# Kernel tuning notes

Measured on AMD Instinct MI355X. Metric: run time of the kernel, lower is better.

## Reference

```python
import math
import jax, jax.numpy as jnp
import numpy as np

B, S, E, H = 4, 1024, 768, 12
HD = E // H
NUM_BUCKETS, MAX_DIST = 320, 800


def setup_inputs() -> dict:
    key = jax.random.key(0)
    ks = jax.random.split(key, 8)
    w = lambda k, sh: jax.random.normal(k, sh, jnp.float32) * 0.02
    return {
        "hidden_states": jax.random.normal(ks[0], (B, S, E), jnp.float32),
        "q_w": w(ks[1], (E, E)), "q_b": jnp.zeros((E,), jnp.float32),
        "k_w": w(ks[2], (E, E)), "k_b": jnp.zeros((E,), jnp.float32),
        "v_w": w(ks[3], (E, E)), "v_b": jnp.zeros((E,), jnp.float32),
        "out_w": w(ks[4], (E, E)), "out_b": jnp.zeros((E,), jnp.float32),
        "gru_const": jnp.ones((1, H, 1, 1), jnp.float32),
        "gru_w": w(ks[5], (8, HD)), "gru_b": jnp.zeros((8,), jnp.float32),
        "rel_embed": w(ks[6], (NUM_BUCKETS, H)),
    }


def _relative_positions_bucket(rel):
    # rel: (S, S) int32, rel = memory_pos - context_pos
    nb = NUM_BUCKETS // 2
    buckets = (rel > 0).astype(jnp.int32) * nb
    rel = jnp.abs(rel)
    max_exact = nb // 2
    is_small = rel < max_exact
    large = jnp.log(rel.astype(jnp.float32) / max_exact)
    large = large / math.log(MAX_DIST / max_exact) * (nb - max_exact)
    large = (max_exact + large).astype(jnp.int32)
    large = jnp.minimum(large, nb - 1)
    return buckets + jnp.where(is_small, rel, large)


def _compute_position_bias(rel_embed):
    pos = jnp.arange(S, dtype=jnp.int32)
    rel = pos[None, :] - pos[:, None]              # (S, S)
    bucket = _relative_positions_bucket(rel)       # (S, S) int32
    return rel_embed[bucket].transpose(2, 0, 1)    # (H, S, S)


def reference(hidden_states, q_w, q_b, k_w, k_b, v_w, v_b, out_w, out_b,
              gru_const, gru_w, gru_b, rel_embed):
    position_bias = _compute_position_bias(rel_embed)          # (H, S, S)

    # gated relative-position bias
    ghs = hidden_states.reshape(B, S, H, HD).transpose(0, 2, 1, 3)   # (B,H,S,HD)
    proj = jnp.einsum("bhsd,ed->bhse", ghs, gru_w) + gru_b           # (B,H,S,8)
    proj = proj.reshape(B, H, S, 2, 4).sum(-1)                       # (B,H,S,2)
    gates = jax.nn.sigmoid(proj)
    gate_a, gate_b = gates[..., 0:1], gates[..., 1:2]                # (B,H,S,1)
    gate = gate_a * (gate_b * gru_const - 1.0) + 2.0                 # (B,H,S,1)
    gated_bias = gate[..., None, :, 0][..., None] * 0  # placeholder removed below
    gated_bias = gate * position_bias[None]                          # (B,H,S,S)

    scaling = HD ** -0.5
    q = (hidden_states @ q_w.T + q_b).reshape(B, S, H, HD).transpose(0, 2, 1, 3) * scaling
    k = (hidden_states @ k_w.T + k_b).reshape(B, S, H, HD).transpose(0, 2, 1, 3)
    v = (hidden_states @ v_w.T + v_b).reshape(B, S, H, HD).transpose(0, 2, 1, 3)

    scores = jnp.einsum("bhqd,bhkd->bhqk", q, k) + gated_bias
    attn = jax.nn.softmax(scores, axis=-1)
    ctx = jnp.einsum("bhqk,bhkd->bhqd", attn, v)                     # (B,H,S,HD)
    ctx = ctx.transpose(0, 2, 1, 3).reshape(B, S, E)
    attn_output = ctx @ out_w.T + out_b
    return attn_output, position_bias
```

## Files before the change

### kernel.cpp

```cpp
#include <hip/hip_runtime.h>

typedef unsigned short u16;
typedef __attribute__((ext_vector_type(4))) unsigned short u16x4;
typedef __attribute__((ext_vector_type(8))) short s8v;
typedef __attribute__((ext_vector_type(4))) float f4v;

#define BB 4
#define SS 1024
#define EE 768
#define HH 12
#define DD 64

#define NHS (BB * SS * EE)
#define NW  (EE * EE)
#define LOG2E 1.4426950408889634f

static __device__ __forceinline__ u16 f2bf(float x){
  unsigned int u = __float_as_uint(x);
  u += 0x7fffu + ((u >> 16) & 1u);
  return (u16)(u >> 16);
}
static __device__ __forceinline__ unsigned cvt_pk_bf16(float lo, float hi){
  unsigned r;
  asm("v_cvt_pk_bf16_f32 %0, %1, %2" : "=v"(r) : "v"(lo), "v"(hi));
  return r;
}
static __device__ __forceinline__ void stage16(const u16* g, u16* l){
  __builtin_amdgcn_global_load_lds(
      (const __attribute__((address_space(1))) void*)g,
      (__attribute__((address_space(3))) void*)l, 16, 0, 0);
}

__global__ __launch_bounds__(256) void cvt_kernel(const float* __restrict__ hs,
                                                  const float* __restrict__ qw,
                                                  const float* __restrict__ kw,
                                                  const float* __restrict__ vw,
                                                  const float* __restrict__ ow,
                                                  u16* __restrict__ dst){
  size_t e = ((size_t)blockIdx.x * 256 + threadIdx.x) * 8;
  const float* src;
  if      (e < (size_t)NHS)            src = hs + e;
  else if (e < (size_t)NHS + NW)       src = qw + (e - NHS);
  else if (e < (size_t)NHS + 2 * NW)   src = kw + (e - NHS - NW);
  else if (e < (size_t)NHS + 3 * NW)   src = vw + (e - NHS - 2 * (size_t)NW);
  else                                 src = ow + (e - NHS - 3 * (size_t)NW);
  f4v v0 = *(const f4v*)src, v1 = *(const f4v*)(src + 4);
  s8v o;
  #pragma unroll
  for (int i = 0; i < 4; i++){ o[i] = (short)f2bf(v0[i]); o[4 + i] = (short)f2bf(v1[i]); }
  size_t row = e / EE;
  int k = (int)(e - row * EE);
  size_t d = row * EE + (size_t)(k ^ (((int)row & 7) << 3));
  *(s8v*)(dst + d) = o;
}

__global__ __launch_bounds__(256) void tbl_kernel(const float* __restrict__ rel_embed,
                                                  float* __restrict__ tbl){
  int id = blockIdx.x * 256 + threadIdx.x;
  int h = id >> 11, r = id & 2047;
  float v = 0.f;
  if (r < 2047){
    int rel = r - 1023;
    int bucket = (rel > 0) ? 160 : 0;
    int a = rel < 0 ? -rel : rel;
    int idx;
    if (a < 80) idx = a;
    else {
      float t = logf((float)a / 80.0f);
      t = t / 2.302585092994046f * 80.0f;
      int lg = (int)(80.0f + t);
      idx = lg < 159 ? lg : 159;
    }
    v = rel_embed[(idx + bucket) * HH + h];
  }
  tbl[id] = v;
}

__global__ __launch_bounds__(256) void pb_kernel(const float* __restrict__ tbl,
                                                 float* __restrict__ pb){
  int id = blockIdx.x * 256 + threadIdx.x;
  int i = id >> 8, j = (id & 255) * 4;
  int base = j - i + 1023;
  #pragma unroll
  for (int h = 0; h < HH; h++){
    const float* th = tbl + h * 2048;
    f4v v;
    #pragma unroll
    for (int jj = 0; jj < 4; jj++) v[jj] = th[base + jj];
    __builtin_nontemporal_store(v, (f4v*)&pb[(size_t)h * (SS * SS) + (size_t)i * SS + j]);
  }
}

__global__ __launch_bounds__(256) void gate_kernel(const float* __restrict__ hs,
                                                   const float* __restrict__ gru_w,
                                                   const float* __restrict__ gru_b,
                                                   const float* __restrict__ gru_c,
                                                   float* __restrict__ gate){
  int wid = blockIdx.x * 4 + (threadIdx.x >> 6);
  int lane = threadIdx.x & 63;
  int s = wid & (SS - 1);
  int bh = wid >> 10;
  int h = bh % HH, b = bh / HH;
  float x = hs[(size_t)(b * SS + s) * EE + h * DD + lane];
  float w0 = gru_w[lane] + gru_w[64 + lane] + gru_w[128 + lane] + gru_w[192 + lane];
  float w1 = gru_w[256 + lane] + gru_w[320 + lane] + gru_w[384 + lane] + gru_w[448 + lane];
  float y0 = x * w0, y1 = x * w1;
  #pragma unroll
  for (int off = 1; off < 64; off <<= 1){
    y0 += __shfl_xor(y0, off);
    y1 += __shfl_xor(y1, off);
  }
  if (lane == 0){
    float s0 = y0 + gru_b[0] + gru_b[1] + gru_b[2] + gru_b[3];
    float s1 = y1 + gru_b[4] + gru_b[5] + gru_b[6] + gru_b[7];
    float ga = 1.f / (1.f + __expf(-s0));
    float gb = 1.f / (1.f + __expf(-s1));
    gate[wid] = ga * (gb * gru_c[h] - 1.0f) + 2.0f;
  }
}

template<int EP>
static __device__ __forceinline__ void gemm_body(const u16* __restrict__ A,
                                                 const u16* __restrict__ Bw,
                                                 const float* __restrict__ bias,
                                                 void* __restrict__ Cp,
                                                 float scale, int m0, int n0){
  __shared__ __align__(16) u16 a_s[128 * 64];
  __shared__ __align__(16) u16 b_s[128 * 64];
  const int t = threadIdx.x;
  const int wave = t >> 6, lane = t & 63;
  const int lr = lane & 15, lg = lane >> 4;
  const int wm = (wave >> 1) * 64, wn = (wave & 1) * 64;
  const int srow = lane >> 3;
  const int scol = (lane & 7) * 8;
  const int swz = (lr & 7) << 3;

  const f4v zero = {0.f, 0.f, 0.f, 0.f};
  f4v acc[4][4];
  #pragma unroll
  for (int i = 0; i < 4; i++)
    #pragma unroll
    for (int j = 0; j < 4; j++) acc[i][j] = zero;

  for (int k0 = 0; k0 < EE; k0 += 64){
    if (k0) __syncthreads();
    #pragma unroll
    for (int i = 0; i < 4; i++){
      const int chunk = i * 4 + wave;
      const int r = chunk * 8 + srow;
      stage16(A  + (size_t)(m0 + r) * EE + k0 + scol, &a_s[chunk * 512]);
      stage16(Bw + (size_t)(n0 + r) * EE + k0 + scol, &b_s[chunk * 512]);
    }
    __syncthreads();
    #pragma unroll
    for (int kk = 0; kk < 2; kk++){
      const int cbase = (kk * 32 + lg * 8) ^ swz;
      s8v af[4], bf[4];
      #pragma unroll
      for (int i = 0; i < 4; i++){
        af[i] = *(const s8v*)&a_s[(wm + i * 16 + lr) * 64 + cbase];
        bf[i] = *(const s8v*)&b_s[(wn + i * 16 + lr) * 64 + cbase];
      }
      #pragma unroll
      for (int i = 0; i < 4; i++)
        #pragma unroll
        for (int j = 0; j < 4; j++)
          acc[i][j] = __builtin_amdgcn_mfma_f32_16x16x32_bf16(af[i], bf[j], acc[i][j], 0, 0, 0);
    }
  }

  #pragma unroll
  for (int ii = 0; ii < 4; ii++){
    const int row0 = m0 + wm + ii * 16 + lg * 4;
    const int bb = row0 >> 10;
    const int s0 = row0 & (SS - 1);
    #pragma unroll
    for (int j = 0; j < 4; j++){
      const int col = n0 + wn + j * 16 + lr;
      const float bv = bias[col];
      if (EP == 0){
        const int h = col >> 6, dim = col & 63;
        const int bh = bb * HH + h;
        u16* dst = (u16*)Cp + ((size_t)((bh * 64 + (s0 >> 4)) * 2 + (dim >> 5))) * 512
                   + ((dim >> 3) & 3) * 128 + (s0 & 15) * 8 + (dim & 7);
        #pragma unroll
        for (int r = 0; r < 4; r++)
          dst[r * 8] = f2bf((acc[ii][j][r] + bv) * scale);
      } else if (EP == 2){
        const int h = col >> 6, dim = col & 63;
        const int bh = bb * HH + h;
        u16x4 pk;
        #pragma unroll
        for (int r = 0; r < 4; r++) pk[r] = f2bf(acc[ii][j][r] + bv);
        *(u16x4*)((u16*)Cp + ((size_t)(((bh * 16 + (s0 >> 6)) * 2 + ((s0 >> 5) & 1)) * 4 + (dim >> 4))) * 512
                  + ((s0 >> 3) & 3) * 128 + (dim & 15) * 8 + (s0 & 7)) = pk;
      } else {
        #pragma unroll
        for (int r = 0; r < 4; r++)
          ((float*)Cp)[(size_t)(row0 + r) * EE + col] = acc[ii][j][r] + bv;
      }
    }
  }
}

__global__ __launch_bounds__(256) void gemm_qkv(const u16* __restrict__ A,
                                                const u16* __restrict__ wqkv,
                                                const float* __restrict__ bq,
                                                const float* __restrict__ bk,
                                                const float* __restrict__ bv,
                                                u16* __restrict__ qo,
                                                u16* __restrict__ ko,
                                                u16* __restrict__ vo){
  const int z = blockIdx.z;
  if (z == 2)
    gemm_body<2>(A, wqkv + 2 * (size_t)NW, bv, vo, 1.0f, blockIdx.x * 128, blockIdx.y * 128);
  else
    gemm_body<0>(A, wqkv + (size_t)z * NW, z ? bk : bq, z ? ko : qo,
                 z ? 1.0f : 0.125f * LOG2E, blockIdx.x * 128, blockIdx.y * 128);
}

__global__ __launch_bounds__(256) void gemm_out(const u16* __restrict__ A,
                                                const u16* __restrict__ Bw,
                                                const float* __restrict__ bias,
                                                float* __restrict__ Cp){
  gemm_body<1>(A, Bw, bias, Cp, 1.0f, blockIdx.x * 128, blockIdx.y * 128);
}

__global__ __launch_bounds__(256) void attn_kernel(const u16* __restrict__ qpack,
                                                   const u16* __restrict__ kpack,
                                                   const u16* __restrict__ vpack,
                                                   const float* __restrict__ gate,
                                                   const float* __restrict__ tbl,
                                                   u16* __restrict__ ctx){
  __shared__ __align__(16) float tbl_s[2048];
  __shared__ __align__(16) u16 kv_s[2][8192];
  __shared__ __align__(16) u16 p_s[4][16][72];
  const int t = threadIdx.x, wave = t >> 6, lane = t & 63;
  const int lr = lane & 15, lg = lane >> 4;
  const int h = blockIdx.y, b = blockIdx.z;
  const int bh = b * HH + h;
  const int q0w = blockIdx.x * 64 + wave * 16;
  {
    const float* th = tbl + h * 2048 + t * 8;
    *(f4v*)&tbl_s[t * 8]     = *(const f4v*)th;
    *(f4v*)&tbl_s[t * 8 + 4] = *(const f4v*)(th + 4);
  }
  const u16* qp = qpack + ((size_t)(bh * 64 + blockIdx.x * 4 + wave)) * 1024 + lane * 8;
  const s8v qf0 = *(const s8v*)qp;
  const s8v qf1 = *(const s8v*)(qp + 512);
  const float gt = gate[(size_t)bh * SS + q0w + lr] * LOG2E;

  const u16* kbase = kpack + (size_t)bh * 65536;
  const u16* vbase = vpack + (size_t)bh * 65536;
  const int so = wave * 1024 + lane * 8;

  stage16(kbase + so,        &kv_s[0][wave * 1024]);
  stage16(kbase + so + 512,  &kv_s[0][wave * 1024 + 512]);
  stage16(vbase + so,        &kv_s[0][4096 + wave * 1024]);
  stage16(vbase + so + 512,  &kv_s[0][4096 + wave * 1024 + 512]);
  __syncthreads();

  const f4v zero = {0.f, 0.f, 0.f, 0.f};
  f4v o[4];
  #pragma unroll
  for (int d = 0; d < 4; d++) o[d] = zero;
  float m = -1e30f, l = 0.f;
  const int tb_off = 1023 - q0w;
  const int voff = lg * 4 - lr;

  for (int kt = 0; kt < 16; kt++){
    const int cur = kt & 1;
    if (kt < 15){
      const u16* kg = kbase + (kt + 1) * 4096;
      const u16* vg = vbase + (kt + 1) * 4096;
      u16* kl = &kv_s[cur ^ 1][wave * 1024];
      u16* vl = &kv_s[cur ^ 1][4096 + wave * 1024];
      stage16(kg + so,       kl);
      stage16(kg + so + 512, kl + 512);
      stage16(vg + so,       vl);
      stage16(vg + so + 512, vl + 512);
    }
    const u16* kl = &kv_s[cur][0];
    const u16* vl = &kv_s[cur][4096];
    s8v kf0[4], kf1[4], vf0[4], vf1[4];
    #pragma unroll
    for (int n = 0; n < 4; n++){
      kf0[n] = *(const s8v*)&kl[n * 1024 + lane * 8];
      kf1[n] = *(const s8v*)&kl[n * 1024 + 512 + lane * 8];
    }
    #pragma unroll
    for (int d = 0; d < 4; d++){
      vf0[d] = *(const s8v*)&vl[d * 512 + lane * 8];
      vf1[d] = *(const s8v*)&vl[2048 + d * 512 + lane * 8];
    }
    f4v sf[4];
    __builtin_amdgcn_s_setprio(1);
    #pragma unroll
    for (int n = 0; n < 4; n++){
      f4v z = zero;
      z = __builtin_amdgcn_mfma_f32_16x16x32_bf16(kf0[n], qf0, z, 0, 0, 0);
      z = __builtin_amdgcn_mfma_f32_16x16x32_bf16(kf1[n], qf1, z, 0, 0, 0);
      sf[n] = z;
    }
    __builtin_amdgcn_s_setprio(0);
    #pragma unroll
    for (int n = 0; n < 4; n++){
      const float* tp = &tbl_s[kt * 64 + n * 16 + tb_off + voff];
      #pragma unroll
      for (int r = 0; r < 4; r++)
        sf[n][r] += gt * tp[r];
    }
    float lm = fmaxf(fmaxf(fmaxf(sf[0][0], sf[0][1]), fmaxf(sf[0][2], sf[0][3])),
                     fmaxf(fmaxf(sf[1][0], sf[1][1]), fmaxf(sf[1][2], sf[1][3])));
    lm = fmaxf(lm, fmaxf(fmaxf(fmaxf(sf[2][0], sf[2][1]), fmaxf(sf[2][2], sf[2][3])),
                         fmaxf(fmaxf(sf[3][0], sf[3][1]), fmaxf(sf[3][2], sf[3][3]))));
    if (__any(lm - m > 8.0f)){
      float gm = fmaxf(lm, __shfl_xor(lm, 16));
      gm = fmaxf(gm, __shfl_xor(gm, 32));
      float nm = fmaxf(m, gm);
      float sc = exp2f(m - nm);
      m = nm;
      l *= sc;
      float scq[4];
      #pragma unroll
      for (int r = 0; r < 4; r++) scq[r] = __shfl(sc, lg * 4 + r);
      #pragma unroll
      for (int d = 0; d < 4; d++)
        #pragma unroll
        for (int r = 0; r < 4; r++) o[d][r] *= scq[r];
    }
    float ps = 0.f;
    #pragma unroll
    for (int n = 0; n < 4; n++){
      #pragma unroll
      for (int r = 0; r < 4; r++){
        float p = exp2f(sf[n][r] - m);
        sf[n][r] = p;
        ps += p;
      }
    }
    l += ps;
    #pragma unroll
    for (int n = 0; n < 4; n++){
      unsigned pk0 = cvt_pk_bf16(sf[n][0], sf[n][1]);
      unsigned pk1 = cvt_pk_bf16(sf[n][2], sf[n][3]);
      u16* prow = &p_s[wave][lr][n * 16 + lg * 4];
      *(unsigned*)prow       = pk0;
      *(unsigned*)(prow + 2) = pk1;
    }
    const s8v pf0 = *(const s8v*)&p_s[wave][lr][lg * 8];
    const s8v pf1 = *(const s8v*)&p_s[wave][lr][32 + lg * 8];
    __builtin_amdgcn_s_setprio(1);
    #pragma unroll
    for (int d = 0; d < 4; d++){
      o[d] = __builtin_amdgcn_mfma_f32_16x16x32_bf16(pf0, vf0[d], o[d], 0, 0, 0);
      o[d] = __builtin_amdgcn_mfma_f32_16x16x32_bf16(pf1, vf1[d], o[d], 0, 0, 0);
    }
    __builtin_amdgcn_s_setprio(0);
    __syncthreads();
  }
  l += __shfl_xor(l, 16);
  l += __shfl_xor(l, 32);
  float rl = 1.0f / l;
  float linv[4];
  #pragma unroll
  for (int r = 0; r < 4; r++) linv[r] = __shfl(rl, lg * 4 + r);
  #pragma unroll
  for (int d = 0; d < 4; d++)
    #pragma unroll
    for (int r = 0; r < 4; r++){
      float val = o[d][r] * linv[r];
      const int row = q0w + lg * 4 + r;
      const int col = (h * DD + d * 16 + lr) ^ ((row & 7) << 3);
      ctx[(size_t)(b * SS + row) * EE + col] = f2bf(val);
    }
}

extern "C" void kernel_launch(void* const* d_in, const int* in_sizes, int n_in,
                              void* d_out, int out_size, void* d_ws, size_t ws_size,
                              hipStream_t stream){
  const float* hs    = (const float*)d_in[0];
  const float* q_w   = (const float*)d_in[1];
  const float* q_b   = (const float*)d_in[2];
  const float* k_w   = (const float*)d_in[3];
  const float* k_b   = (const float*)d_in[4];
  const float* v_w   = (const float*)d_in[5];
  const float* v_b   = (const float*)d_in[6];
  const float* o_w   = (const float*)d_in[7];
  const float* o_b   = (const float*)d_in[8];
  const float* gru_c = (const float*)d_in[9];
  const float* gru_w = (const float*)d_in[10];
  const float* gru_b = (const float*)d_in[11];
  const float* rel   = (const float*)d_in[12];

  float* out0 = (float*)d_out;
  float* pb   = out0 + (size_t)BB * SS * EE;

  char* w = (char*)d_ws;
  u16* qpk  = (u16*)w;  w += (size_t)NHS * 2;
  u16* kpk  = (u16*)w;  w += (size_t)NHS * 2;
  u16* vpk  = (u16*)w;  w += (size_t)NHS * 2;
  u16* cvt  = (u16*)w;  w += ((size_t)NHS + 4 * (size_t)NW) * 2;
  float* gate = (float*)w; w += (size_t)BB * HH * SS * 4;
  float* tbl  = (float*)w;

  u16* hs_bf  = cvt;
  u16* wqkv   = cvt + NHS;
  u16* ow_bf  = cvt + NHS + 3 * (size_t)NW;

  cvt_kernel<<<(NHS + 4 * NW) / (256 * 8), 256, 0, stream>>>(hs, q_w, k_w, v_w, o_w, cvt);
  tbl_kernel<<<(HH * 2048) / 256, 256, 0, stream>>>(rel, tbl);
  gate_kernel<<<(BB * HH * SS) / 4, 256, 0, stream>>>(hs, gru_w, gru_b, gru_c, gate);
  gemm_qkv<<<dim3(32, 6, 3), 256, 0, stream>>>(hs_bf, wqkv, q_b, k_b, v_b, qpk, kpk, vpk);
  attn_kernel<<<dim3(SS / 64, HH, BB), 256, 0, stream>>>(qpk, kpk, vpk, gate, tbl, hs_bf);
  gemm_out<<<dim3(32, 6), 256, 0, stream>>>(hs_bf, ow_bf, o_b, out0);
  pb_kernel<<<(SS * SS / 4) / 256, 256, 0, stream>>>(tbl, pb);
}
```

Measured before the change: 116.5 us.

## Merge prep kernels and fuse position-bias output write into attention epilogue

```diff
diff --git a/kernel.cpp b/kernel.cpp
--- a/kernel.cpp
+++ b/kernel.cpp
@@ -31,91 +31,76 @@
       (__attribute__((address_space(3))) void*)l, 16, 0, 0);
 }
 
-__global__ __launch_bounds__(256) void cvt_kernel(const float* __restrict__ hs,
-                                                  const float* __restrict__ qw,
-                                                  const float* __restrict__ kw,
-                                                  const float* __restrict__ vw,
-                                                  const float* __restrict__ ow,
-                                                  u16* __restrict__ dst){
-  size_t e = ((size_t)blockIdx.x * 256 + threadIdx.x) * 8;
-  const float* src;
-  if      (e < (size_t)NHS)            src = hs + e;
-  else if (e < (size_t)NHS + NW)       src = qw + (e - NHS);
-  else if (e < (size_t)NHS + 2 * NW)   src = kw + (e - NHS - NW);
-  else if (e < (size_t)NHS + 3 * NW)   src = vw + (e - NHS - 2 * (size_t)NW);
-  else                                 src = ow + (e - NHS - 3 * (size_t)NW);
-  f4v v0 = *(const f4v*)src, v1 = *(const f4v*)(src + 4);
-  s8v o;
-  #pragma unroll
-  for (int i = 0; i < 4; i++){ o[i] = (short)f2bf(v0[i]); o[4 + i] = (short)f2bf(v1[i]); }
-  size_t row = e / EE;
-  int k = (int)(e - row * EE);
-  size_t d = row * EE + (size_t)(k ^ (((int)row & 7) << 3));
-  *(s8v*)(dst + d) = o;
-}
-
-__global__ __launch_bounds__(256) void tbl_kernel(const float* __restrict__ rel_embed,
-                                                  float* __restrict__ tbl){
-  int id = blockIdx.x * 256 + threadIdx.x;
-  int h = id >> 11, r = id & 2047;
-  float v = 0.f;
-  if (r < 2047){
-    int rel = r - 1023;
-    int bucket = (rel > 0) ? 160 : 0;
-    int a = rel < 0 ? -rel : rel;
-    int idx;
-    if (a < 80) idx = a;
-    else {
-      float t = logf((float)a / 80.0f);
-      t = t / 2.302585092994046f * 80.0f;
-      int lg = (int)(80.0f + t);
-      idx = lg < 159 ? lg : 159;
-    }
-    v = rel_embed[(idx + bucket) * HH + h];
-  }
-  tbl[id] = v;
-}
-
-__global__ __launch_bounds__(256) void pb_kernel(const float* __restrict__ tbl,
-                                                 float* __restrict__ pb){
-  int id = blockIdx.x * 256 + threadIdx.x;
-  int i = id >> 8, j = (id & 255) * 4;
-  int base = j - i + 1023;
-  #pragma unroll
-  for (int h = 0; h < HH; h++){
-    const float* th = tbl + h * 2048;
-    f4v v;
-    #pragma unroll
-    for (int jj = 0; jj < 4; jj++) v[jj] = th[base + jj];
-    __builtin_nontemporal_store(v, (f4v*)&pb[(size_t)h * (SS * SS) + (size_t)i * SS + j]);
-  }
-}
-
-__global__ __launch_bounds__(256) void gate_kernel(const float* __restrict__ hs,
+__global__ __launch_bounds__(256) void prep_kernel(const float* __restrict__ hs,
+                                                   const float* __restrict__ qw,
+                                                   const float* __restrict__ kw,
+                                                   const float* __restrict__ vw,
+                                                   const float* __restrict__ ow,
+                                                   u16* __restrict__ dst,
+                                                   const float* __restrict__ rel_embed,
+                                                   float* __restrict__ tbl,
                                                    const float* __restrict__ gru_w,
                                                    const float* __restrict__ gru_b,
                                                    const float* __restrict__ gru_c,
                                                    float* __restrict__ gate){
-  int wid = blockIdx.x * 4 + (threadIdx.x >> 6);
-  int lane = threadIdx.x & 63;
-  int s = wid & (SS - 1);
-  int bh = wid >> 10;
-  int h = bh % HH, b = bh / HH;
-  float x = hs[(size_t)(b * SS + s) * EE + h * DD + lane];
-  float w0 = gru_w[lane] + gru_w[64 + lane] + gru_w[128 + lane] + gru_w[192 + lane];
-  float w1 = gru_w[256 + lane] + gru_w[320 + lane] + gru_w[384 + lane] + gru_w[448 + lane];
-  float y0 = x * w0, y1 = x * w1;
-  #pragma unroll
-  for (int off = 1; off < 64; off <<= 1){
-    y0 += __shfl_xor(y0, off);
-    y1 += __shfl_xor(y1, off);
-  }
-  if (lane == 0){
-    float s0 = y0 + gru_b[0] + gru_b[1] + gru_b[2] + gru_b[3];
-    float s1 = y1 + gru_b[4] + gru_b[5] + gru_b[6] + gru_b[7];
-    float ga = 1.f / (1.f + __expf(-s0));
-    float gb = 1.f / (1.f + __expf(-s1));
-    gate[wid] = ga * (gb * gru_c[h] - 1.0f) + 2.0f;
+  const int bid = blockIdx.x;
+  if (bid < 2688){
+    size_t e = ((size_t)bid * 256 + threadIdx.x) * 8;
+    const float* src;
+    if      (e < (size_t)NHS)            src = hs + e;
+    else if (e < (size_t)NHS + NW)       src = qw + (e - NHS);
+    else if (e < (size_t)NHS + 2 * NW)   src = kw + (e - NHS - NW);
+    else if (e < (size_t)NHS + 3 * NW)   src = vw + (e - NHS - 2 * (size_t)NW);
+    else                                 src = ow + (e - NHS - 3 * (size_t)NW);
+    f4v v0 = *(const f4v*)src, v1 = *(const f4v*)(src + 4);
+    s8v o;
+    #pragma unroll
+    for (int i = 0; i < 4; i++){ o[i] = (short)f2bf(v0[i]); o[4 + i] = (short)f2bf(v1[i]); }
+    size_t row = e / EE;
+    int k = (int)(e - row * EE);
+    size_t d = row * EE + (size_t)(k ^ (((int)row & 7) << 3));
+    *(s8v*)(dst + d) = o;
+  } else if (bid < 2784){
+    int id = (bid - 2688) * 256 + threadIdx.x;
+    int h = id >> 11, r = id & 2047;
+    float v = 0.f;
+    if (r < 2047){
+      int rel = r - 1023;
+      int bucket = (rel > 0) ? 160 : 0;
+      int a = rel < 0 ? -rel : rel;
+      int idx;
+      if (a < 80) idx = a;
+      else {
+        float t = logf((float)a / 80.0f);
+        t = t / 2.302585092994046f * 80.0f;
+        int lg = (int)(80.0f + t);
+        idx = lg < 159 ? lg : 159;
+      }
+      v = rel_embed[(idx + bucket) * HH + h];
+    }
+    tbl[id] = v;
+  } else {
+    int wid = (bid - 2784) * 4 + (threadIdx.x >> 6);
+    int lane = threadIdx.x & 63;
+    int s = wid & (SS - 1);
+    int bh = wid >> 10;
+    int h = bh % HH, b = bh / HH;
+    float x = hs[(size_t)(b * SS + s) * EE + h * DD + lane];
+    float w0 = gru_w[lane] + gru_w[64 + lane] + gru_w[128 + lane] + gru_w[192 + lane];
+    float w1 = gru_w[256 + lane] + gru_w[320 + lane] + gru_w[384 + lane] + gru_w[448 + lane];
+    float y0 = x * w0, y1 = x * w1;
+    #pragma unroll
+    for (int off = 1; off < 64; off <<= 1){
+      y0 += __shfl_xor(y0, off);
+      y1 += __shfl_xor(y1, off);
+    }
+    if (lane == 0){
+      float s0 = y0 + gru_b[0] + gru_b[1] + gru_b[2] + gru_b[3];
+      float s1 = y1 + gru_b[4] + gru_b[5] + gru_b[6] + gru_b[7];
+      float ga = 1.f / (1.f + __expf(-s0));
+      float gb = 1.f / (1.f + __expf(-s1));
+      gate[wid] = ga * (gb * gru_c[h] - 1.0f) + 2.0f;
+    }
   }
 }
 
@@ -231,7 +216,8 @@
                                                    const u16* __restrict__ vpack,
                                                    const float* __restrict__ gate,
                                                    const float* __restrict__ tbl,
-                                                   u16* __restrict__ ctx){
+                                                   u16* __restrict__ ctx,
+                                                   float* __restrict__ pb){
   __shared__ __align__(16) float tbl_s[2048];
   __shared__ __align__(16) u16 kv_s[2][8192];
   __shared__ __align__(16) u16 p_s[4][16][72];
@@ -374,6 +360,21 @@
       const int col = (h * DD + d * 16 + lr) ^ ((row & 7) << 3);
       ctx[(size_t)(b * SS + row) * EE + col] = f2bf(val);
     }
+  {
+    float* pbh = pb + (size_t)h * (SS * SS);
+    const int i0 = (blockIdx.x * 4 + b) * 16;
+    #pragma unroll 4
+    for (int rr = 0; rr < 16; rr++){
+      const int i = i0 + rr;
+      const int base = 1023 - i + t * 4;
+      f4v v;
+      v[0] = tbl_s[base + 0];
+      v[1] = tbl_s[base + 1];
+      v[2] = tbl_s[base + 2];
+      v[3] = tbl_s[base + 3];
+      __builtin_nontemporal_store(v, (f4v*)&pbh[(size_t)i * SS + t * 4]);
+    }
+  }
 }
 
 extern "C" void kernel_launch(void* const* d_in, const int* in_sizes, int n_in,
@@ -408,11 +409,9 @@
   u16* wqkv   = cvt + NHS;
   u16* ow_bf  = cvt + NHS + 3 * (size_t)NW;
 
-  cvt_kernel<<<(NHS + 4 * NW) / (256 * 8), 256, 0, stream>>>(hs, q_w, k_w, v_w, o_w, cvt);
-  tbl_kernel<<<(HH * 2048) / 256, 256, 0, stream>>>(rel, tbl);
-  gate_kernel<<<(BB * HH * SS) / 4, 256, 0, stream>>>(hs, gru_w, gru_b, gru_c, gate);
+  prep_kernel<<<15072, 256, 0, stream>>>(hs, q_w, k_w, v_w, o_w, cvt,
+                                         rel, tbl, gru_w, gru_b, gru_c, gate);
   gemm_qkv<<<dim3(32, 6, 3), 256, 0, stream>>>(hs_bf, wqkv, q_b, k_b, v_b, qpk, kpk, vpk);
-  attn_kernel<<<dim3(SS / 64, HH, BB), 256, 0, stream>>>(qpk, kpk, vpk, gate, tbl, hs_bf);
+  attn_kernel<<<dim3(SS / 64, HH, BB), 256, 0, stream>>>(qpk, kpk, vpk, gate, tbl, hs_bf, pb);
   gemm_out<<<dim3(32, 6), 256, 0, stream>>>(hs_bf, ow_bf, o_b, out0);
-  pb_kernel<<<(SS * SS / 4) / 256, 256, 0, stream>>>(tbl, pb);
-}
+}
```

Result: faster. 104.1 us (-10.6%).
